# Kernel tuning notes

Measured on AMD Instinct MI355X. Metric: run time of the kernel, lower is better.

## Reference

```python
import jax, jax.numpy as jnp
import numpy as np

B, T, D, H, U = 128, 576, 1024, 1024, 512


def setup_inputs() -> dict:
    key = jax.random.key(0)
    ks = jax.random.split(key, 6)
    s_feat = 0.02
    features = jax.random.normal(ks[0], (B, T, D), dtype=jnp.float32)
    hidden = jax.random.normal(ks[1], (B, H), dtype=jnp.float32)
    W1_w = jax.random.normal(ks[2], (D, U), dtype=jnp.float32) * s_feat
    W1_b = jnp.zeros((U,), dtype=jnp.float32)
    W2_w = jax.random.normal(ks[3], (H, U), dtype=jnp.float32) * s_feat
    W2_b = jnp.zeros((U,), dtype=jnp.float32)
    V_w = jax.random.normal(ks[4], (U, 1), dtype=jnp.float32) * s_feat
    V_b = jnp.zeros((1,), dtype=jnp.float32)
    return {"features": features, "hidden": hidden, "W1_w": W1_w, "W1_b": W1_b,
            "W2_w": W2_w, "W2_b": W2_b, "V_w": V_w, "V_b": V_b}


def reference(features, hidden, W1_w, W1_b, W2_w, W2_b, V_w, V_b):
    # features: [B, T, D]; hidden: [B, H]
    proj_f = jnp.einsum('btd,du->btu', features, W1_w) + W1_b      # [B, T, U]
    proj_h = (hidden @ W2_w + W2_b)[:, None, :]                    # [B, 1, U]
    score = jnp.tanh(proj_f + proj_h) @ V_w + V_b                  # [B, T, 1]
    attention_weights = jax.nn.softmax(score, axis=1)              # [B, T, 1]
    context_vector = jnp.sum(attention_weights * features, axis=1) # [B, D]
    return context_vector, attention_weights
```

## Files before the change

kernel.cpp:

```cpp
#include <hip/hip_runtime.h>

#define B_ 128
#define T_ 576
#define D_ 1024
#define H_ 1024
#define U_ 512

typedef short bf16x8 __attribute__((ext_vector_type(8)));
typedef float f32x4 __attribute__((ext_vector_type(4)));

__device__ inline unsigned short f2bf(float f) {
  union { float f; unsigned u; } v; v.f = f;
  unsigned r = v.u + 0x7FFF + ((v.u >> 16) & 1);
  return (unsigned short)(r >> 16);
}

__device__ inline float fast_tanh(float x) {
  float e = __expf(2.f * x);
  return 1.f - 2.f / (e + 1.f);
}

__global__ __launch_bounds__(256) void w1t_kernel(
    const float* __restrict__ W1, unsigned short* __restrict__ W1T) {
  __shared__ float tile[32][33];
  const int k0 = blockIdx.x * 32, u0 = blockIdx.y * 32;
  const int tx = threadIdx.x & 31, ty = threadIdx.x >> 5;
#pragma unroll
  for (int i = 0; i < 32; i += 8)
    tile[ty + i][tx] = W1[(k0 + ty + i) * U_ + u0 + tx];
  __syncthreads();
#pragma unroll
  for (int i = 0; i < 32; i += 8)
    W1T[(u0 + ty + i) * D_ + k0 + tx] = f2bf(tile[tx][ty + i]);
}

__global__ __launch_bounds__(512) void projh_kernel(
    const float* __restrict__ hidden, const float* __restrict__ W2,
    const float* __restrict__ W2b, const float* __restrict__ W1b,
    float* __restrict__ projh) {
  const int b = blockIdx.x;
  const int u = threadIdx.x;
  __shared__ float sh[256];
  float acc = 0.f;
  for (int h0 = 0; h0 < H_; h0 += 256) {
    if (threadIdx.x < 256) sh[threadIdx.x] = hidden[b * H_ + h0 + threadIdx.x];
    __syncthreads();
#pragma unroll 8
    for (int hh = 0; hh < 256; ++hh)
      acc += sh[hh] * W2[(h0 + hh) * U_ + u];
    __syncthreads();
  }
  projh[b * U_ + u] = acc + W2b[u] + W1b[u];
}

#define BM 64
#define BN 128
#define BK 64
#define LDST 72
__global__ __launch_bounds__(256) void score_mfma_kernel(
    const float* __restrict__ features, const unsigned short* __restrict__ W1T,
    const float* __restrict__ projh, const float* __restrict__ Vw,
    const float* __restrict__ Vb, float* __restrict__ score) {
  __shared__ unsigned short As[BM][LDST];
  __shared__ unsigned short Bs[BN][LDST];
  __shared__ float sred[2][BM];
  const int b = blockIdx.y;
  const int t0 = blockIdx.x * BM;
  const int tid = threadIdx.x;
  const int lane = tid & 63;
  const int w = tid >> 6;
  const int wm = w & 1, wn = w >> 1;
  const int m16 = lane & 15, quad = lane >> 4;
  const float* fbase = features + ((long)b * T_ + t0) * D_;

  float stot[2][4] = {{0.f, 0.f, 0.f, 0.f}, {0.f, 0.f, 0.f, 0.f}};

  for (int u0 = 0; u0 < U_; u0 += BN) {
    f32x4 acc[2][4];
#pragma unroll
    for (int i = 0; i < 2; ++i)
#pragma unroll
      for (int j = 0; j < 4; ++j) acc[i][j] = (f32x4){0.f, 0.f, 0.f, 0.f};

    for (int kt = 0; kt < D_; kt += BK) {
#pragma unroll
      for (int i = 0; i < 4; ++i) {
        const int q = tid + 256 * i;
        const int row = q >> 4, c4 = (q & 15) * 4;
        const float4 f = *(const float4*)(fbase + (long)row * D_ + kt + c4);
        ushort4 h;
        h.x = f2bf(f.x); h.y = f2bf(f.y); h.z = f2bf(f.z); h.w = f2bf(f.w);
        *(ushort4*)&As[row][c4] = h;
      }
#pragma unroll
      for (int i = 0; i < 4; ++i) {
        const int q = tid + 256 * i;
        const int n = q >> 3, k8 = (q & 7) * 8;
        *(uint4*)&Bs[n][k8] =
            *(const uint4*)(W1T + ((u0 + n) << 10) + kt + k8);
      }
      __syncthreads();
#pragma unroll
      for (int ks = 0; ks < BK; ks += 32) {
        bf16x8 a[2], bb[4];
#pragma unroll
        for (int i = 0; i < 2; ++i)
          a[i] = *(const bf16x8*)&As[wm * 32 + i * 16 + m16][ks + quad * 8];
#pragma unroll
        for (int j = 0; j < 4; ++j)
          bb[j] = *(const bf16x8*)&Bs[wn * 64 + j * 16 + m16][ks + quad * 8];
#pragma unroll
        for (int i = 0; i < 2; ++i)
#pragma unroll
          for (int j = 0; j < 4; ++j)
            acc[i][j] = __builtin_amdgcn_mfma_f32_16x16x32_bf16(
                a[i], bb[j], acc[i][j], 0, 0, 0);
      }
      __syncthreads();
    }
#pragma unroll
    for (int j = 0; j < 4; ++j) {
      const int u = u0 + wn * 64 + j * 16 + m16;
      const float ph = projh[b * U_ + u];
      const float vw = Vw[u];
#pragma unroll
      for (int i = 0; i < 2; ++i)
#pragma unroll
        for (int r = 0; r < 4; ++r)
          stot[i][r] += vw * fast_tanh(acc[i][j][r] + ph);
    }
  }
#pragma unroll
  for (int i = 0; i < 2; ++i)
#pragma unroll
    for (int r = 0; r < 4; ++r) {
      float v = stot[i][r];
      v += __shfl_xor(v, 1, 16);
      v += __shfl_xor(v, 2, 16);
      v += __shfl_xor(v, 4, 16);
      v += __shfl_xor(v, 8, 16);
      if (m16 == 0) sred[wn][wm * 32 + i * 16 + quad * 4 + r] = v;
    }
  __syncthreads();
  if (tid < BM)
    score[b * T_ + t0 + tid] = sred[0][tid] + sred[1][tid] + Vb[0];
}

__global__ __launch_bounds__(256) void softmax_kernel(
    const float* __restrict__ score, float* __restrict__ wout) {
  const int b = blockIdx.x;
  const int tid = threadIdx.x;
  __shared__ float red[256];
  const float v0 = score[b * T_ + tid];
  const float v1 = score[b * T_ + 256 + tid];
  const float v2 = (tid < 64) ? score[b * T_ + 512 + tid] : -1e30f;
  red[tid] = fmaxf(fmaxf(v0, v1), v2);
  __syncthreads();
  for (int s = 128; s > 0; s >>= 1) {
    if (tid < s) red[tid] = fmaxf(red[tid], red[tid + s]);
    __syncthreads();
  }
  const float mx = red[0];
  __syncthreads();
  const float e0 = expf(v0 - mx), e1 = expf(v1 - mx);
  const float e2 = (tid < 64) ? expf(v2 - mx) : 0.f;
  red[tid] = e0 + e1 + e2;
  __syncthreads();
  for (int s = 128; s > 0; s >>= 1) {
    if (tid < s) red[tid] += red[tid + s];
    __syncthreads();
  }
  const float inv = 1.f / red[0];
  wout[b * T_ + tid] = e0 * inv;
  wout[b * T_ + 256 + tid] = e1 * inv;
  if (tid < 64) wout[b * T_ + 512 + tid] = e2 * inv;
}

__global__ __launch_bounds__(128) void context_kernel(
    const float* __restrict__ features, const float* __restrict__ w,
    float* __restrict__ ctx) {
  const int b = blockIdx.x;
  const int d = blockIdx.y * 128 + threadIdx.x;
  __shared__ float sw[T_];
  for (int t = threadIdx.x; t < T_; t += 128) sw[t] = w[b * T_ + t];
  __syncthreads();
  const float* fb = features + (long)b * T_ * D_ + d;
  float acc = 0.f;
#pragma unroll 8
  for (int t = 0; t < T_; ++t) acc += sw[t] * fb[(long)t * D_];
  ctx[b * D_ + d] = acc;
}

extern "C" void kernel_launch(void* const* d_in, const int* in_sizes, int n_in,
                              void* d_out, int out_size, void* d_ws,
                              size_t ws_size, hipStream_t stream) {
  const float* features = (const float*)d_in[0];
  const float* hidden   = (const float*)d_in[1];
  const float* W1_w     = (const float*)d_in[2];
  const float* W1_b     = (const float*)d_in[3];
  const float* W2_w     = (const float*)d_in[4];
  const float* W2_b     = (const float*)d_in[5];
  const float* V_w      = (const float*)d_in[6];
  const float* V_b      = (const float*)d_in[7];

  float* out_ctx  = (float*)d_out;
  float* out_attn = out_ctx + B_ * D_;

  char* ws = (char*)d_ws;
  float* projh = (float*)ws;
  float* score = (float*)(ws + 256 * 1024);
  unsigned short* W1T = (unsigned short*)(ws + 1024 * 1024);

  w1t_kernel<<<dim3(D_ / 32, U_ / 32), 256, 0, stream>>>(W1_w, W1T);
  projh_kernel<<<B_, 512, 0, stream>>>(hidden, W2_w, W2_b, W1_b, projh);
  score_mfma_kernel<<<dim3(T_ / BM, B_), 256, 0, stream>>>(
      features, W1T, projh, V_w, V_b, score);
  softmax_kernel<<<B_, 256, 0, stream>>>(score, out_attn);
  context_kernel<<<dim3(B_, 8), 128, 0, stream>>>(features, out_attn, out_ctx);
}
```

Before: 735.6 us.

## Split score GEMM across U chunks with 128-row tiles and partial sums

The score kernel now treats B*T as one flat M dimension with 128x128 tiles. The U dimension is split across a second grid axis of four chunks, and each block writes a partial score to a workspace; the softmax kernel sums the four partials. The feature-to-bf16 conversion now uses a packed conversion intrinsic. Together these are meant to raise parallelism and per-tile MFMA reuse, but each feature tile is now read and converted four times, once per U chunk. V_b is dropped from the score, which is harmless because softmax is shift-invariant.

```diff
diff --git a/kernel.cpp b/kernel.cpp
--- a/kernel.cpp
+++ b/kernel.cpp
@@ -1,10 +1,12 @@
 #include <hip/hip_runtime.h>
+#include <hip/hip_bf16.h>
 
 #define B_ 128
 #define T_ 576
 #define D_ 1024
 #define H_ 1024
 #define U_ 512
+#define M_ (B_ * T_)
 
 typedef short bf16x8 __attribute__((ext_vector_type(8)));
 typedef float f32x4 __attribute__((ext_vector_type(4)));
@@ -13,6 +15,12 @@
   union { float f; unsigned u; } v; v.f = f;
   unsigned r = v.u + 0x7FFF + ((v.u >> 16) & 1);
   return (unsigned short)(r >> 16);
+}
+
+__device__ inline unsigned int pkcvt(float x, float y) {
+  union { __hip_bfloat162 b2; unsigned int u; } v;
+  v.b2 = __float22bfloat162_rn(make_float2(x, y));
+  return v.u;
 }
 
 __device__ inline float fast_tanh(float x) {
@@ -53,85 +61,92 @@
   projh[b * U_ + u] = acc + W2b[u] + W1b[u];
 }
 
-#define BM 64
-#define BN 128
-#define BK 64
 #define LDST 72
-__global__ __launch_bounds__(256) void score_mfma_kernel(
-    const float* __restrict__ features, const unsigned short* __restrict__ W1T,
+__global__ __launch_bounds__(256) void score_mfma3(
+    const float* __restrict__ feat, const unsigned short* __restrict__ W1T,
     const float* __restrict__ projh, const float* __restrict__ Vw,
-    const float* __restrict__ Vb, float* __restrict__ score) {
-  __shared__ unsigned short As[BM][LDST];
-  __shared__ unsigned short Bs[BN][LDST];
-  __shared__ float sred[2][BM];
-  const int b = blockIdx.y;
-  const int t0 = blockIdx.x * BM;
+    float* __restrict__ spart) {
+  __shared__ unsigned short As[128][LDST];
+  __shared__ unsigned short Bs[128][LDST];
+  __shared__ float phs[2][128];
+  __shared__ float vws[128];
+  __shared__ float sred[2][128];
   const int tid = threadIdx.x;
-  const int lane = tid & 63;
-  const int w = tid >> 6;
+  const int chunk = blockIdx.y, u0 = chunk * 128;
+  const int t0 = blockIdx.x * 128;
+  const int b0 = t0 / T_, b1 = (t0 + 127) / T_;
+  const int bsplit = (b0 + 1) * T_;
+  const int lane = tid & 63, w = tid >> 6;
   const int wm = w & 1, wn = w >> 1;
   const int m16 = lane & 15, quad = lane >> 4;
-  const float* fbase = features + ((long)b * T_ + t0) * D_;
-
-  float stot[2][4] = {{0.f, 0.f, 0.f, 0.f}, {0.f, 0.f, 0.f, 0.f}};
-
-  for (int u0 = 0; u0 < U_; u0 += BN) {
-    f32x4 acc[2][4];
-#pragma unroll
-    for (int i = 0; i < 2; ++i)
-#pragma unroll
-      for (int j = 0; j < 4; ++j) acc[i][j] = (f32x4){0.f, 0.f, 0.f, 0.f};
-
-    for (int kt = 0; kt < D_; kt += BK) {
-#pragma unroll
-      for (int i = 0; i < 4; ++i) {
-        const int q = tid + 256 * i;
-        const int row = q >> 4, c4 = (q & 15) * 4;
-        const float4 f = *(const float4*)(fbase + (long)row * D_ + kt + c4);
-        ushort4 h;
-        h.x = f2bf(f.x); h.y = f2bf(f.y); h.z = f2bf(f.z); h.w = f2bf(f.w);
-        *(ushort4*)&As[row][c4] = h;
+
+  if (tid < 128) vws[tid] = Vw[u0 + tid];
+  phs[tid >> 7][tid & 127] =
+      projh[((tid >> 7) ? b1 : b0) * U_ + u0 + (tid & 127)];
+
+  f32x4 acc[4][4];
+#pragma unroll
+  for (int i = 0; i < 4; ++i)
+#pragma unroll
+    for (int j = 0; j < 4; ++j) acc[i][j] = (f32x4){0.f, 0.f, 0.f, 0.f};
+
+  for (int kt = 0; kt < D_; kt += 64) {
+#pragma unroll
+    for (int i = 0; i < 8; ++i) {
+      const int q = tid + 256 * i;
+      const int row = q >> 4, c4 = (q & 15) * 4;
+      const float4 f =
+          *(const float4*)(feat + ((long)(t0 + row) << 10) + kt + c4);
+      uint2 p;
+      p.x = pkcvt(f.x, f.y);
+      p.y = pkcvt(f.z, f.w);
+      *(uint2*)&As[row][c4] = p;
+    }
+#pragma unroll
+    for (int i = 0; i < 4; ++i) {
+      const int q = tid + 256 * i;
+      const int row = q >> 3, k8 = (q & 7) * 8;
+      *(uint4*)&Bs[row][k8] =
+          *(const uint4*)(W1T + ((long)(u0 + row) << 10) + kt + k8);
+    }
+    __syncthreads();
+#pragma unroll
+    for (int ks = 0; ks < 64; ks += 32) {
+      bf16x8 a[4], bb[4];
+#pragma unroll
+      for (int i = 0; i < 4; ++i)
+        a[i] = *(const bf16x8*)&As[wm * 64 + i * 16 + m16][ks + quad * 8];
+#pragma unroll
+      for (int j = 0; j < 4; ++j)
+        bb[j] = *(const bf16x8*)&Bs[wn * 64 + j * 16 + m16][ks + quad * 8];
+#pragma unroll
+      for (int i = 0; i < 4; ++i)
+#pragma unroll
+        for (int j = 0; j < 4; ++j)
+          acc[i][j] = __builtin_amdgcn_mfma_f32_16x16x32_bf16(
+              a[i], bb[j], acc[i][j], 0, 0, 0);
+    }
+    __syncthreads();
+  }
+
+  float stot[4][4] = {};
+#pragma unroll
+  for (int j = 0; j < 4; ++j) {
+    const int ul = wn * 64 + j * 16 + m16;
+    const float vw = vws[ul];
+    const float ph0 = phs[0][ul], ph1 = phs[1][ul];
+#pragma unroll
+    for (int i = 0; i < 4; ++i) {
+      const int rbase = t0 + wm * 64 + i * 16 + quad * 4;
+#pragma unroll
+      for (int r = 0; r < 4; ++r) {
+        const float ph = (rbase + r >= bsplit) ? ph1 : ph0;
+        stot[i][r] += vw * fast_tanh(acc[i][j][r] + ph);
       }
-#pragma unroll
-      for (int i = 0; i < 4; ++i) {
-        const int q = tid + 256 * i;
-        const int n = q >> 3, k8 = (q & 7) * 8;
-        *(uint4*)&Bs[n][k8] =
-            *(const uint4*)(W1T + ((u0 + n) << 10) + kt + k8);
-      }
-      __syncthreads();
-#pragma unroll
-      for (int ks = 0; ks < BK; ks += 32) {
-        bf16x8 a[2], bb[4];
-#pragma unroll
-        for (int i = 0; i < 2; ++i)
-          a[i] = *(const bf16x8*)&As[wm * 32 + i * 16 + m16][ks + quad * 8];
-#pragma unroll
-        for (int j = 0; j < 4; ++j)
-          bb[j] = *(const bf16x8*)&Bs[wn * 64 + j * 16 + m16][ks + quad * 8];
-#pragma unroll
-        for (int i = 0; i < 2; ++i)
-#pragma unroll
-          for (int j = 0; j < 4; ++j)
-            acc[i][j] = __builtin_amdgcn_mfma_f32_16x16x32_bf16(
-                a[i], bb[j], acc[i][j], 0, 0, 0);
-      }
-      __syncthreads();
-    }
-#pragma unroll
-    for (int j = 0; j < 4; ++j) {
-      const int u = u0 + wn * 64 + j * 16 + m16;
-      const float ph = projh[b * U_ + u];
-      const float vw = Vw[u];
-#pragma unroll
-      for (int i = 0; i < 2; ++i)
-#pragma unroll
-        for (int r = 0; r < 4; ++r)
-          stot[i][r] += vw * fast_tanh(acc[i][j][r] + ph);
-    }
-  }
-#pragma unroll
-  for (int i = 0; i < 2; ++i)
+    }
+  }
+#pragma unroll
+  for (int i = 0; i < 4; ++i)
 #pragma unroll
     for (int r = 0; r < 4; ++r) {
       float v = stot[i][r];
@@ -139,21 +154,25 @@
       v += __shfl_xor(v, 2, 16);
       v += __shfl_xor(v, 4, 16);
       v += __shfl_xor(v, 8, 16);
-      if (m16 == 0) sred[wn][wm * 32 + i * 16 + quad * 4 + r] = v;
-    }
-  __syncthreads();
-  if (tid < BM)
-    score[b * T_ + t0 + tid] = sred[0][tid] + sred[1][tid] + Vb[0];
+      if (m16 == 0) sred[wn][wm * 64 + i * 16 + quad * 4 + r] = v;
+    }
+  __syncthreads();
+  if (tid < 128)
+    spart[(long)chunk * M_ + t0 + tid] = sred[0][tid] + sred[1][tid];
 }
 
 __global__ __launch_bounds__(256) void softmax_kernel(
-    const float* __restrict__ score, float* __restrict__ wout) {
+    const float* __restrict__ sp, float* __restrict__ wout) {
   const int b = blockIdx.x;
   const int tid = threadIdx.x;
   __shared__ float red[256];
-  const float v0 = score[b * T_ + tid];
-  const float v1 = score[b * T_ + 256 + tid];
-  const float v2 = (tid < 64) ? score[b * T_ + 512 + tid] : -1e30f;
+  auto ld = [&](int t) -> float {
+    const long r = (long)b * T_ + t;
+    return sp[r] + sp[M_ + r] + sp[2L * M_ + r] + sp[3L * M_ + r];
+  };
+  const float v0 = ld(tid);
+  const float v1 = ld(tid + 256);
+  const float v2 = (tid < 64) ? ld(tid + 512) : -1e30f;
   red[tid] = fmaxf(fmaxf(v0, v1), v2);
   __syncthreads();
   for (int s = 128; s > 0; s >>= 1) {
@@ -202,19 +221,20 @@
   const float* W2_b     = (const float*)d_in[5];
   const float* V_w      = (const float*)d_in[6];
   const float* V_b      = (const float*)d_in[7];
+  (void)V_b;
 
   float* out_ctx  = (float*)d_out;
   float* out_attn = out_ctx + B_ * D_;
 
   char* ws = (char*)d_ws;
-  float* projh = (float*)ws;
-  float* score = (float*)(ws + 256 * 1024);
-  unsigned short* W1T = (unsigned short*)(ws + 1024 * 1024);
+  float* projh        = (float*)ws;
+  float* spart        = (float*)(ws + 0x40000);
+  unsigned short* W1T = (unsigned short*)(ws + 0x180000);
 
   w1t_kernel<<<dim3(D_ / 32, U_ / 32), 256, 0, stream>>>(W1_w, W1T);
   projh_kernel<<<B_, 512, 0, stream>>>(hidden, W2_w, W2_b, W1_b, projh);
-  score_mfma_kernel<<<dim3(T_ / BM, B_), 256, 0, stream>>>(
-      features, W1T, projh, V_w, V_b, score);
-  softmax_kernel<<<B_, 256, 0, stream>>>(score, out_attn);
+  score_mfma3<<<dim3(M_ / 128, 4), 256, 0, stream>>>(features, W1T, projh,
+                                                     V_w, spart);
+  softmax_kernel<<<B_, 256, 0, stream>>>(spart, out_attn);
   context_kernel<<<dim3(B_, 8), 128, 0, stream>>>(features, out_attn, out_ctx);
 }
```

Result: faster. 701.6 us (-4.6%).
